# Performance work log

Hardware: AMD Instinct MI355X
Metric: run time of the kernel (lower is better)

The kernel has to match this reference:

```python
import jax, jax.numpy as jnp
import numpy as np

B, T, D_IN, D = 32, 40, 1024, 400


def _offset(level, length):
    return level * length - level * (level - 1) // 2


def _unit(h):
    return h / (jnp.linalg.norm(h, axis=-1, keepdims=True) + 1e-8)


def _inside_index(length):
    idx = {}
    for level in range(1, length):
        L = length - level
        li = np.zeros((L, level), np.int32)
        ri = np.zeros((L, level), np.int32)
        for pos in range(L):
            for k in range(level):
                li[pos, k] = _offset(k, length) + pos
                ri[pos, k] = _offset(level - k - 1, length) + pos + k + 1
        idx[level] = (li, ri)
    return idx


def _outside_index(length):
    idx = {}
    for level in range(length - 2, -1, -1):
        L = length - level
        N = length - level - 1
        pi = np.zeros((L, N), np.int32)
        si = np.zeros((L, N), np.int32)
        for pos in range(L):
            c = 0
            for j in range(pos):  # sibling on the left of this span
                pi[pos, c] = _offset(level + j + 1, length) + pos - j - 1
                si[pos, c] = _offset(j, length) + pos - j - 1
                c += 1
            for j in range(L - 1 - pos):  # sibling on the right
                pi[pos, c] = _offset(level + j + 1, length) + pos
                si[pos, c] = _offset(j, length) + pos + level + 1
                c += 1
        idx[level] = (pi, si)
    return idx


def _diora_forward(x, W_leaf, b_leaf, W_in, b_in, S_in, W_out, b_out, S_out, root_h):
    Bb, length, _ = x.shape
    size = W_leaf.shape[1]
    ncells = length * (length + 1) // 2
    in_idx = _inside_index(length)
    out_idx = _outside_index(length)

    h_in = jnp.zeros((Bb, ncells, size), x.dtype)
    s_in = jnp.zeros((Bb, ncells), x.dtype)
    h_out = jnp.zeros((Bb, ncells, size), x.dtype)
    s_out = jnp.zeros((Bb, ncells), x.dtype)

    # leaf transform + unit normalize (level 0 of inside chart)
    leaf = _unit(jax.nn.relu(x @ W_leaf + b_leaf))
    h_in = h_in.at[:, :length].set(leaf)

    # inside pass: bottom-up CKY levels
    for level in range(1, length):
        L = length - level
        off = _offset(level, length)
        li, ri = in_idx[level]
        hl = h_in[:, li]  # [B, L, level, D]
        hr = h_in[:, ri]
        hc = jax.nn.relu(jnp.einsum('blkd,df->blkf', jnp.concatenate([hl, hr], -1), W_in) + b_in)
        sb = jnp.einsum('blkd,de,blke->blk', hl, S_in, hr) + s_in[:, li] + s_in[:, ri]
        p = jax.nn.softmax(sb, axis=-1)
        h_in = h_in.at[:, off:off + L].set(_unit(jnp.einsum('blk,blkd->bld', p, hc)))
        s_in = s_in.at[:, off:off + L].set(jnp.sum(p * sb, axis=-1))

    # outside pass: root init then top-down
    root = _unit(root_h)[None, None, :]
    h_out = h_out.at[:, -1:].set(jnp.broadcast_to(root, (Bb, 1, size)))
    for level in range(length - 2, -1, -1):
        L = length - level
        off = _offset(level, length)
        pi, si = out_idx[level]
        hp = h_out[:, pi]  # [B, L, N, D] parent outside
        hs = h_in[:, si]   # [B, L, N, D] sibling inside
        hc = jax.nn.relu(jnp.einsum('blnd,df->blnf', jnp.concatenate([hp, hs], -1), W_out) + b_out)
        sb = jnp.einsum('blnd,de,blne->bln', hp, S_out, hs) + s_out[:, pi] + s_in[:, si]
        p = jax.nn.softmax(sb, axis=-1)
        h_out = h_out.at[:, off:off + L].set(_unit(jnp.einsum('bln,blnd->bld', p, hc)))
        s_out = s_out.at[:, off:off + L].set(jnp.sum(p * sb, axis=-1))

    # pack chart: [B, ncells, 2*(D+1)]
    return jnp.concatenate([h_in, s_in[..., None], h_out, s_out[..., None]], axis=-1)


def setup_inputs() -> dict:
    key = jax.random.key(0)
    ks = jax.random.split(key, 10)
    return {
        'x': jax.random.normal(ks[0], (B, T, D_IN), jnp.float32),
        'W_leaf': jax.random.normal(ks[1], (D_IN, D), jnp.float32),
        'b_leaf': jax.random.normal(ks[2], (D,), jnp.float32),
        'W_in': jax.random.normal(ks[3], (2 * D, D), jnp.float32),
        'b_in': jax.random.normal(ks[4], (D,), jnp.float32),
        'S_in': jax.random.normal(ks[5], (D, D), jnp.float32),
        'W_out': jax.random.normal(ks[6], (2 * D, D), jnp.float32),
        'b_out': jax.random.normal(ks[7], (D,), jnp.float32),
        'S_out': jax.random.normal(ks[8], (D, D), jnp.float32),
        'root_h': jax.random.normal(ks[9], (D,), jnp.float32),
    }


def reference(x, W_leaf, b_leaf, W_in, b_in, S_in, W_out, b_out, S_out, root_h):
    return _diora_forward(x, W_leaf, b_leaf, W_in, b_in, S_in, W_out, b_out, S_out, root_h)
```

## Files before the change

### kernel.cpp

```cpp
#include <hip/hip_runtime.h>
#include <hip/hip_bf16.h>
#include <math.h>


#define TLEN 40
#define DD 400
#define NCELL 820
#define STR 802

typedef short bf16x8 __attribute__((ext_vector_type(8)));
typedef float f32x4 __attribute__((ext_vector_type(4)));

__host__ __device__ __forceinline__ int coff(int l) { return l * TLEN - (l * (l - 1)) / 2; }
__device__ __forceinline__ float bf2f(unsigned short u) {
    return __uint_as_float(((unsigned)u) << 16);
}
__device__ __forceinline__ unsigned short f2bf(float v) {
    __hip_bfloat16 h = __float2bfloat16(v);
    return *reinterpret_cast<unsigned short*>(&h);
}

__global__ __launch_bounds__(256)
void prep_weights(const float* __restrict__ Win, const float* __restrict__ Sin,
                  const float* __restrict__ Wout, const float* __restrict__ Sout,
                  const float* __restrict__ Wl,
                  unsigned short* __restrict__ WinT, unsigned short* __restrict__ WoutT,
                  unsigned short* __restrict__ WlT)
{
    int n = blockIdx.x;
    if (n < 2400) {
        const float* src; int col; unsigned short* dst;
        if (n < 1200) {
            dst = WinT + (size_t)n * 400;
            if (n < 400)      { src = Win;             col = n; }
            else if (n < 800) { src = Win + 400 * 400; col = n - 400; }
            else              { src = Sin;             col = n - 800; }
        } else {
            int m = n - 1200;
            dst = WoutT + (size_t)m * 400;
            if (m < 400)      { src = Wout;             col = m; }
            else if (m < 800) { src = Sout;             col = m - 400; }
            else              { src = Wout + 400 * 400; col = m - 800; }
        }
        for (int k = threadIdx.x; k < 400; k += 256)
            dst[k] = f2bf(src[(size_t)k * 400 + col]);
    } else {
        int m = n - 2400;
        unsigned short* dst = WlT + (size_t)m * 1024;
        for (int k = threadIdx.x; k < 1024; k += 256)
            dst[k] = f2bf(Wl[(size_t)k * 400 + m]);
    }
}

__global__ __launch_bounds__(256)
void mgemm(const unsigned short* __restrict__ A, const unsigned short* __restrict__ WT,
           unsigned short* __restrict__ Cb, unsigned short* __restrict__ Cc,
           int M, int N, int L, int cb, int co_b, int nsplit)
{
    __shared__ unsigned short As[64][40];
    __shared__ unsigned short Bs[128][40];
    const int tid = threadIdx.x;
    const int bm = blockIdx.x, bn = blockIdx.y;
    const int w = tid >> 6, lane = tid & 63;
    const int l15 = lane & 15, kb = (lane >> 4) * 8;

    const int ar = tid >> 2, ach = (tid & 3) * 8;
    const int rg = bm * 64 + ar;
    const unsigned short* Ap = nullptr;
    if (rg < M) { int b = rg / L, p = rg - b * L;
                  Ap = A + ((size_t)(b * NCELL) + cb + p) * 400; }

    const int bcol = tid & 127, bh = (tid >> 7) * 16;
    const int ng = bn * 128 + bcol;
    const unsigned short* Bp = (ng < N) ? WT + (size_t)ng * 400 : nullptr;

    f32x4 acc[4][2];
    #pragma unroll
    for (int r = 0; r < 4; ++r)
        #pragma unroll
        for (int c = 0; c < 2; ++c) { f32x4 z = {0.f, 0.f, 0.f, 0.f}; acc[r][c] = z; }

    for (int k0 = 0; k0 < 400; k0 += 32) {
        int4 av = {0, 0, 0, 0};
        if (Ap && (k0 + ach) < 400) av = *(const int4*)(Ap + k0 + ach);
        int4 bv0 = {0, 0, 0, 0}, bv1 = {0, 0, 0, 0};
        if (Bp && (k0 + bh) < 400) {
            bv0 = *(const int4*)(Bp + k0 + bh);
            bv1 = *(const int4*)(Bp + k0 + bh + 8);
        }
        __syncthreads();
        *(int4*)&As[ar][ach] = av;
        *(int4*)&Bs[bcol][bh] = bv0;
        *(int4*)&Bs[bcol][bh + 8] = bv1;
        __syncthreads();

        bf16x8 af[4], bf[2];
        #pragma unroll
        for (int r = 0; r < 4; ++r) af[r] = *(const bf16x8*)&As[r * 16 + l15][kb];
        #pragma unroll
        for (int c = 0; c < 2; ++c) bf[c] = *(const bf16x8*)&Bs[w * 32 + c * 16 + l15][kb];
        #pragma unroll
        for (int r = 0; r < 4; ++r)
            #pragma unroll
            for (int c = 0; c < 2; ++c)
                acc[r][c] = __builtin_amdgcn_mfma_f32_16x16x32_bf16(af[r], bf[c], acc[r][c], 0, 0, 0);
    }

    const int rowb = (lane >> 4) * 4;
    #pragma unroll
    for (int r = 0; r < 4; ++r) {
        #pragma unroll
        for (int c = 0; c < 2; ++c) {
            int gcol = bn * 128 + w * 32 + c * 16 + l15;
            if (gcol >= N) continue;
            #pragma unroll
            for (int reg = 0; reg < 4; ++reg) {
                int rr = bm * 64 + r * 16 + rowb + reg;
                if (rr >= M) continue;
                int b = rr / L, p = rr - b * L;
                size_t cell = (size_t)(b * NCELL) + cb + p;
                unsigned short v = f2bf(acc[r][c][reg]);
                if (gcol < nsplit) Cb[cell * 800 + co_b + gcol] = v;
                else               Cc[cell * 400 + (gcol - nsplit)] = v;
            }
        }
    }
}

__global__ __launch_bounds__(256)
void mleaf(const float* __restrict__ x, const unsigned short* __restrict__ WlT,
           const float* __restrict__ bias, float* __restrict__ leafS)
{
    __shared__ unsigned short As[64][40];
    __shared__ unsigned short Bs[128][40];
    const int tid = threadIdx.x;
    const int bm = blockIdx.x, bn = blockIdx.y;
    const int w = tid >> 6, lane = tid & 63;
    const int l15 = lane & 15, kb = (lane >> 4) * 8;

    const int ar = tid >> 2, ach = (tid & 3) * 8;
    const float* Ap = x + (size_t)(bm * 64 + ar) * 1024;

    const int bcol = tid & 127, bh = (tid >> 7) * 16;
    const int ng = bn * 128 + bcol;
    const unsigned short* Bp = (ng < 400) ? WlT + (size_t)ng * 1024 : nullptr;

    f32x4 acc[4][2];
    #pragma unroll
    for (int r = 0; r < 4; ++r)
        #pragma unroll
        for (int c = 0; c < 2; ++c) { f32x4 z = {0.f, 0.f, 0.f, 0.f}; acc[r][c] = z; }

    for (int k0 = 0; k0 < 1024; k0 += 32) {
        float4 p0 = *(const float4*)(Ap + k0 + ach);
        float4 p1 = *(const float4*)(Ap + k0 + ach + 4);
        unsigned short av[8];
        av[0] = f2bf(p0.x); av[1] = f2bf(p0.y); av[2] = f2bf(p0.z); av[3] = f2bf(p0.w);
        av[4] = f2bf(p1.x); av[5] = f2bf(p1.y); av[6] = f2bf(p1.z); av[7] = f2bf(p1.w);
        int4 bv0 = {0, 0, 0, 0}, bv1 = {0, 0, 0, 0};
        if (Bp) {
            bv0 = *(const int4*)(Bp + k0 + bh);
            bv1 = *(const int4*)(Bp + k0 + bh + 8);
        }
        __syncthreads();
        *(int4*)&As[ar][ach] = *(const int4*)av;
        *(int4*)&Bs[bcol][bh] = bv0;
        *(int4*)&Bs[bcol][bh + 8] = bv1;
        __syncthreads();

        bf16x8 af[4], bf[2];
        #pragma unroll
        for (int r = 0; r < 4; ++r) af[r] = *(const bf16x8*)&As[r * 16 + l15][kb];
        #pragma unroll
        for (int c = 0; c < 2; ++c) bf[c] = *(const bf16x8*)&Bs[w * 32 + c * 16 + l15][kb];
        #pragma unroll
        for (int r = 0; r < 4; ++r)
            #pragma unroll
            for (int c = 0; c < 2; ++c)
                acc[r][c] = __builtin_amdgcn_mfma_f32_16x16x32_bf16(af[r], bf[c], acc[r][c], 0, 0, 0);
    }

    const int rowb = (lane >> 4) * 4;
    #pragma unroll
    for (int r = 0; r < 4; ++r) {
        #pragma unroll
        for (int c = 0; c < 2; ++c) {
            int gcol = bn * 128 + w * 32 + c * 16 + l15;
            if (gcol >= 400) continue;
            float bv = bias[gcol];
            #pragma unroll
            for (int reg = 0; reg < 4; ++reg) {
                int rr = bm * 64 + r * 16 + rowb + reg;
                leafS[(size_t)rr * 400 + gcol] = fmaxf(acc[r][c][reg] + bv, 0.f);
            }
        }
    }
}

__global__ __launch_bounds__(256)
void unit_leaf(float* obuf, const float* __restrict__ leafS, unsigned short* __restrict__ hHin)
{
    int w = threadIdx.x >> 6, lane = threadIdx.x & 63;
    int r = blockIdx.x * 4 + w;
    int b = r / TLEN, pos = r - b * TLEN;
    const float* t = leafS + (size_t)r * 400;
    float ss = 0.f;
    for (int f = lane; f < DD; f += 64) { float v = t[f]; ss += v * v; }
    #pragma unroll
    for (int o = 32; o; o >>= 1) ss += __shfl_xor(ss, o);
    float rinv = 1.f / (sqrtf(ss) + 1e-8f);
    size_t orow = ((size_t)b * NCELL + pos) * STR;
    size_t hrow = ((size_t)b * NCELL + pos) * 400;
    for (int f = lane; f < DD; f += 64) {
        float v = t[f] * rinv;
        obuf[orow + f] = v;
        hHin[hrow + f] = f2bf(v);
    }
    if (lane == 0) obuf[orow + DD] = 0.f;
}

template<int INSIDE>
__global__ __launch_bounds__(256)
void compose_kernel(int lv, float* obuf, const unsigned short* __restrict__ hAB,
                    const unsigned short* __restrict__ hCb,
                    const unsigned short* __restrict__ hHin,
                    unsigned short* __restrict__ hHw,
                    const float* __restrict__ bias)
{
    const int nk  = INSIDE ? lv : (TLEN - 1 - lv);
    const int b   = blockIdx.x & 31;
    const int pos = blockIdx.x >> 5;
    const int cell = coff(lv) + pos;
    const int tid = threadIdx.x;
    const int sA  = INSIDE ? DD : (STR - 1);

    __shared__ int   o1s[TLEN], o2s[TLEN], c1s[TLEN], h2s[TLEN], q1s[TLEN], q2s[TLEN];
    __shared__ float sbs[TLEN], ps[TLEN];
    __shared__ float bsh[DD];
    __shared__ float hnew[DD];
    __shared__ float red[4];
    __shared__ float sh_snew;

    if (tid < nk) {
        int k = tid, i1, i2;
        if (INSIDE) {
            i1 = coff(k) + pos;
            i2 = coff(lv - k - 1) + pos + k + 1;
        } else {
            if (k < pos) { i1 = coff(lv + k + 1) + pos - k - 1; i2 = coff(k) + pos - k - 1; }
            else         { int j = k - pos; i1 = coff(lv + j + 1) + pos; i2 = coff(j) + pos + lv + 1; }
        }
        o1s[k] = (b * NCELL + i1) * 800;
        o2s[k] = (b * NCELL + i2) * 800 + 400;
        c1s[k] = (b * NCELL + i1) * 400;
        h2s[k] = (b * NCELL + i2) * 400;
        q1s[k] = (b * NCELL + i1) * STR;
        q2s[k] = (b * NCELL + i2) * STR;
    }
    for (int f = tid; f < DD; f += 256) bsh[f] = bias[f];
    __syncthreads();

    {
        const int g = tid >> 4, gl = tid & 15;
        for (int k = g; k < nk; k += 16) {
            const unsigned short* v1 = hCb + c1s[k];
            const unsigned short* v2 = hHin + h2s[k];
            float acc = 0.f;
            for (int j = gl * 4; j < 400; j += 64) {
                ushort4 a = *(const ushort4*)(v1 + j);
                ushort4 c = *(const ushort4*)(v2 + j);
                acc += bf2f(a.x) * bf2f(c.x) + bf2f(a.y) * bf2f(c.y)
                     + bf2f(a.z) * bf2f(c.z) + bf2f(a.w) * bf2f(c.w);
            }
            acc += __shfl_xor(acc, 8);
            acc += __shfl_xor(acc, 4);
            acc += __shfl_xor(acc, 2);
            acc += __shfl_xor(acc, 1);
            if (gl == 0)
                sbs[k] = acc + obuf[q1s[k] + sA] + obuf[q2s[k] + DD];
        }
    }
    __syncthreads();

    if (tid < 64) {
        float v = (tid < nk) ? sbs[tid] : -INFINITY;
        float m = v;
        #pragma unroll
        for (int o = 32; o; o >>= 1) m = fmaxf(m, __shfl_xor(m, o));
        float e = (tid < nk) ? __expf(v - m) : 0.f;
        float s = e;
        #pragma unroll
        for (int o = 32; o; o >>= 1) s += __shfl_xor(s, o);
        float p = e / s;
        if (tid < nk) ps[tid] = p;
        float pv = (tid < nk) ? p * v : 0.f;
        #pragma unroll
        for (int o = 32; o; o >>= 1) pv += __shfl_xor(pv, o);
        if (tid == 0) sh_snew = pv;
    }
    __syncthreads();

    if (tid < 200) {
        const int f = 2 * tid;
        const float bf0 = bsh[f], bf1 = bsh[f + 1];
        float ax = 0.f, ay = 0.f;
        #pragma unroll 4
        for (int k = 0; k < nk; ++k) {
            ushort2 a = *(const ushort2*)(hAB + o1s[k] + f);
            ushort2 c = *(const ushort2*)(hAB + o2s[k] + f);
            float p = ps[k];
            ax += p * fmaxf(bf2f(a.x) + bf2f(c.x) + bf0, 0.f);
            ay += p * fmaxf(bf2f(a.y) + bf2f(c.y) + bf1, 0.f);
        }
        hnew[f] = ax; hnew[f + 1] = ay;
    }
    __syncthreads();

    float ss = 0.f;
    for (int f = tid; f < DD; f += 256) { float v = hnew[f]; ss += v * v; }
    #pragma unroll
    for (int o = 32; o; o >>= 1) ss += __shfl_xor(ss, o);
    if ((tid & 63) == 0) red[tid >> 6] = ss;
    __syncthreads();
    float rinv = 1.f / (sqrtf(red[0] + red[1] + red[2] + red[3]) + 1e-8f);

    const int hoff = INSIDE ? 0 : (DD + 1);
    const int soff = INSIDE ? DD : (STR - 1);
    size_t orow = ((size_t)(b * NCELL) + cell) * STR;
    size_t hrow = ((size_t)(b * NCELL) + cell) * 400;
    for (int f = tid; f < DD; f += 256) {
        float v = hnew[f] * rinv;
        obuf[orow + hoff + f] = v;
        hHw[hrow + f] = f2bf(v);
    }
    if (tid == 0) obuf[orow + soff] = sh_snew;
}

__global__ __launch_bounds__(256)
void root_trans(const float* __restrict__ rooth, const float* __restrict__ Wout,
                const float* __restrict__ Sout,
                unsigned short* __restrict__ hAB, unsigned short* __restrict__ hCb)
{
    const int tid = threadIdx.x;
    __shared__ float u[DD];
    __shared__ float red[4];
    __shared__ float part[4][64];
    float ss = 0.f;
    for (int f = tid; f < DD; f += 256) { float v = rooth[f]; ss += v * v; }
    #pragma unroll
    for (int o = 32; o; o >>= 1) ss += __shfl_xor(ss, o);
    if ((tid & 63) == 0) red[tid >> 6] = ss;
    __syncthreads();
    float rinv = 1.f / (sqrtf(red[0] + red[1] + red[2] + red[3]) + 1e-8f);
    for (int f = tid; f < DD; f += 256) u[f] = rooth[f] * rinv;
    __syncthreads();

    const int w = tid >> 6, lane = tid & 63;
    const int n = blockIdx.x * 64 + lane;
    float acc = 0.f;
    if (n < 800) {
        int mat = n / DD;
        const float* Mp = mat ? Sout : Wout;
        int c = n - mat * DD;
        #pragma unroll 4
        for (int k = w * 100; k < w * 100 + 100; ++k) acc += u[k] * Mp[(size_t)k * DD + c];
    }
    part[w][lane] = acc;
    __syncthreads();
    if (w == 0 && n < 800) {
        float v = part[0][lane] + part[1][lane] + part[2][lane] + part[3][lane];
        unsigned short bv = f2bf(v);
        if (n < 400) {
            for (int b = 0; b < 32; ++b)
                hAB[((size_t)b * NCELL + NCELL - 1) * 800 + n] = bv;
        } else {
            for (int b = 0; b < 32; ++b)
                hCb[((size_t)b * NCELL + NCELL - 1) * 400 + (n - 400)] = bv;
        }
    }
}

__global__ __launch_bounds__(256)
void root_write(const float* __restrict__ rooth, float* obuf)
{
    const int b = blockIdx.x;
    const int tid = threadIdx.x;
    __shared__ float red[4];
    float ss = 0.f;
    for (int f = tid; f < DD; f += 256) { float v = rooth[f]; ss += v * v; }
    #pragma unroll
    for (int o = 32; o; o >>= 1) ss += __shfl_xor(ss, o);
    if ((tid & 63) == 0) red[tid >> 6] = ss;
    __syncthreads();
    float rinv = 1.f / (sqrtf(red[0] + red[1] + red[2] + red[3]) + 1e-8f);
    size_t orow = ((size_t)b * NCELL + NCELL - 1) * STR;
    for (int f = tid; f < DD; f += 256) obuf[orow + DD + 1 + f] = rooth[f] * rinv;
    if (tid == 0) obuf[orow + STR - 1] = 0.f;
}

extern "C" void kernel_launch(void* const* d_in, const int* in_sizes, int n_in,
                              void* d_out, int out_size, void* d_ws, size_t ws_size,
                              hipStream_t stream)
{
    const float* x     = (const float*)d_in[0];
    const float* Wl    = (const float*)d_in[1];
    const float* blf   = (const float*)d_in[2];
    const float* Win   = (const float*)d_in[3];
    const float* bin   = (const float*)d_in[4];
    const float* Sin   = (const float*)d_in[5];
    const float* Wout  = (const float*)d_in[6];
    const float* bout  = (const float*)d_in[7];
    const float* Sout  = (const float*)d_in[8];
    const float* rooth = (const float*)d_in[9];

    float* obuf = (float*)d_out;
    unsigned short* hAB   = (unsigned short*)d_ws;
    unsigned short* hCb   = hAB   + (size_t)32 * NCELL * 800;
    unsigned short* hHin  = hCb   + (size_t)32 * NCELL * 400;
    unsigned short* hHout = hHin  + (size_t)32 * NCELL * 400;
    unsigned short* WinT  = hHout + (size_t)32 * NCELL * 400;
    unsigned short* WoutT = WinT  + (size_t)1200 * 400;
    unsigned short* WlT   = WoutT + (size_t)1200 * 400;
    float* leafS = (float*)(WlT + (size_t)400 * 1024);

    prep_weights<<<2800, 256, 0, stream>>>(Win, Sin, Wout, Sout, Wl, WinT, WoutT, WlT);

    mleaf<<<dim3(20, 4), 256, 0, stream>>>(x, WlT, blf, leafS);
    unit_leaf<<<320, 256, 0, stream>>>(obuf, leafS, hHin);

    for (int lv = 0; lv < TLEN; ++lv) {
        int L = TLEN - lv;
        int cb = coff(lv);
        if (lv > 0)
            compose_kernel<1><<<L * 32, 256, 0, stream>>>(lv, obuf, hAB, hCb, hHin, hHin, bin);
        if (lv < TLEN - 1) {
            int M = L * 32;
            dim3 g((M + 63) / 64, 10);
            mgemm<<<g, 256, 0, stream>>>(hHin, WinT, hAB, hCb, M, 1200, L, cb, 0, 800);
        }
    }

    {
        dim3 g(410, 4);
        mgemm<<<g, 256, 0, stream>>>(hHin, WoutT + (size_t)800 * 400, hAB, hCb,
                                     32 * NCELL, 400, NCELL, 0, 400, 400);
    }
    root_trans<<<13, 256, 0, stream>>>(rooth, Wout, Sout, hAB, hCb);
    root_write<<<32, 256, 0, stream>>>(rooth, obuf);

    for (int lv = TLEN - 2; lv >= 0; --lv) {
        int L = TLEN - lv;
        int cb = coff(lv);
        compose_kernel<0><<<L * 32, 256, 0, stream>>>(lv, obuf, hAB, hCb, hHin, hHout, bout);
        if (lv > 0) {
            int M = L * 32;
            dim3 g((M + 63) / 64, 7);
            mgemm<<<g, 256, 0, stream>>>(hHout, WoutT, hAB, hCb, M, 800, L, cb, 0, 400);
        }
    }
}
```

Measured before the change: 2.142 ms.

## Fuse outside-sibling projection into inside GEMMs, widen K-tile, prefetch compose operands

The outside-pass sibling projection (Wout lower half applied to inside states) is folded into the per-level inside GEMM as a third output segment written to a new hBout buffer. This removes the separate full-chart GEMM. The GEMM K-tile doubles from 32 to 64, so there are fewer barriers per tile at the cost of more LDS. The compose kernel now prefetches the first 8 child rows into shared memory while the score reduction runs, and root_write is merged into root_trans. These changes add an extra workspace buffer and raise per-block register and LDS pressure.

Result: slower. 3.825 ms (+78.6%).

```diff
diff --git a/kernel.cpp b/kernel.cpp
--- a/kernel.cpp
+++ b/kernel.cpp
@@ -24,24 +24,24 @@
 void prep_weights(const float* __restrict__ Win, const float* __restrict__ Sin,
                   const float* __restrict__ Wout, const float* __restrict__ Sout,
                   const float* __restrict__ Wl,
-                  unsigned short* __restrict__ WinT, unsigned short* __restrict__ WoutT,
+                  unsigned short* __restrict__ WinX, unsigned short* __restrict__ WoutT,
                   unsigned short* __restrict__ WlT)
 {
     int n = blockIdx.x;
-    if (n < 2400) {
-        const float* src; int col; unsigned short* dst;
-        if (n < 1200) {
-            dst = WinT + (size_t)n * 400;
-            if (n < 400)      { src = Win;             col = n; }
-            else if (n < 800) { src = Win + 400 * 400; col = n - 400; }
-            else              { src = Sin;             col = n - 800; }
-        } else {
-            int m = n - 1200;
-            dst = WoutT + (size_t)m * 400;
-            if (m < 400)      { src = Wout;             col = m; }
-            else if (m < 800) { src = Sout;             col = m - 400; }
-            else              { src = Wout + 400 * 400; col = m - 800; }
-        }
+    if (n < 1600) {
+        const float* src; int col;
+        if (n < 400)       { src = Win;              col = n; }
+        else if (n < 800)  { src = Win + 400 * 400;  col = n - 400; }
+        else if (n < 1200) { src = Sin;              col = n - 800; }
+        else               { src = Wout + 400 * 400; col = n - 1200; }
+        unsigned short* dst = WinX + (size_t)n * 400;
+        for (int k = threadIdx.x; k < 400; k += 256)
+            dst[k] = f2bf(src[(size_t)k * 400 + col]);
+    } else if (n < 2400) {
+        int m = n - 1600;
+        const float* src = (m < 400) ? Wout : Sout;
+        int col = (m < 400) ? m : m - 400;
+        unsigned short* dst = WoutT + (size_t)m * 400;
         for (int k = threadIdx.x; k < 400; k += 256)
             dst[k] = f2bf(src[(size_t)k * 400 + col]);
     } else {
@@ -55,24 +55,34 @@
 __global__ __launch_bounds__(256)
 void mgemm(const unsigned short* __restrict__ A, const unsigned short* __restrict__ WT,
            unsigned short* __restrict__ Cb, unsigned short* __restrict__ Cc,
-           int M, int N, int L, int cb, int co_b, int nsplit)
-{
-    __shared__ unsigned short As[64][40];
-    __shared__ unsigned short Bs[128][40];
+           unsigned short* __restrict__ Cd,
+           int M, int N, int L, int cb, int ns1, int ns2)
+{
+    __shared__ unsigned short As[64][72];
+    __shared__ unsigned short Bs[128][72];
     const int tid = threadIdx.x;
     const int bm = blockIdx.x, bn = blockIdx.y;
     const int w = tid >> 6, lane = tid & 63;
     const int l15 = lane & 15, kb = (lane >> 4) * 8;
 
-    const int ar = tid >> 2, ach = (tid & 3) * 8;
-    const int rg = bm * 64 + ar;
-    const unsigned short* Ap = nullptr;
-    if (rg < M) { int b = rg / L, p = rg - b * L;
-                  Ap = A + ((size_t)(b * NCELL) + cb + p) * 400; }
-
-    const int bcol = tid & 127, bh = (tid >> 7) * 16;
-    const int ng = bn * 128 + bcol;
-    const unsigned short* Bp = (ng < N) ? WT + (size_t)ng * 400 : nullptr;
+    int arow[2] = { tid >> 3, (tid + 256) >> 3 };
+    const int akc = (tid & 7) * 8;
+    const unsigned short* Aps[2];
+    #pragma unroll
+    for (int i = 0; i < 2; ++i) {
+        int rg = bm * 64 + arow[i];
+        if (rg < M) { int b = rg / L, p = rg - b * L;
+                      Aps[i] = A + ((size_t)(b * NCELL) + cb + p) * 400; }
+        else Aps[i] = nullptr;
+    }
+    int bcol[4];
+    const unsigned short* Bps[4];
+    #pragma unroll
+    for (int i = 0; i < 4; ++i) {
+        bcol[i] = (tid + i * 256) >> 3;
+        int ng = bn * 128 + bcol[i];
+        Bps[i] = (ng < N) ? WT + (size_t)ng * 400 : nullptr;
+    }
 
     f32x4 acc[4][2];
     #pragma unroll
@@ -80,30 +90,39 @@
         #pragma unroll
         for (int c = 0; c < 2; ++c) { f32x4 z = {0.f, 0.f, 0.f, 0.f}; acc[r][c] = z; }
 
-    for (int k0 = 0; k0 < 400; k0 += 32) {
-        int4 av = {0, 0, 0, 0};
-        if (Ap && (k0 + ach) < 400) av = *(const int4*)(Ap + k0 + ach);
-        int4 bv0 = {0, 0, 0, 0}, bv1 = {0, 0, 0, 0};
-        if (Bp && (k0 + bh) < 400) {
-            bv0 = *(const int4*)(Bp + k0 + bh);
-            bv1 = *(const int4*)(Bp + k0 + bh + 8);
+    for (int k0 = 0; k0 < 400; k0 += 64) {
+        int4 av[2], bv[4];
+        #pragma unroll
+        for (int i = 0; i < 2; ++i) {
+            int4 z = {0, 0, 0, 0};
+            av[i] = (Aps[i] && (k0 + akc) < 400) ? *(const int4*)(Aps[i] + k0 + akc) : z;
+        }
+        #pragma unroll
+        for (int i = 0; i < 4; ++i) {
+            int4 z = {0, 0, 0, 0};
+            bv[i] = (Bps[i] && (k0 + akc) < 400) ? *(const int4*)(Bps[i] + k0 + akc) : z;
         }
         __syncthreads();
-        *(int4*)&As[ar][ach] = av;
-        *(int4*)&Bs[bcol][bh] = bv0;
-        *(int4*)&Bs[bcol][bh + 8] = bv1;
+        #pragma unroll
+        for (int i = 0; i < 2; ++i) *(int4*)&As[arow[i]][akc] = av[i];
+        #pragma unroll
+        for (int i = 0; i < 4; ++i) *(int4*)&Bs[bcol[i]][akc] = bv[i];
         __syncthreads();
 
-        bf16x8 af[4], bf[2];
-        #pragma unroll
-        for (int r = 0; r < 4; ++r) af[r] = *(const bf16x8*)&As[r * 16 + l15][kb];
-        #pragma unroll
-        for (int c = 0; c < 2; ++c) bf[c] = *(const bf16x8*)&Bs[w * 32 + c * 16 + l15][kb];
-        #pragma unroll
-        for (int r = 0; r < 4; ++r)
+        #pragma unroll
+        for (int ks = 0; ks < 64; ks += 32) {
+            if (k0 + ks >= 400) break;
+            bf16x8 af[4], bf[2];
             #pragma unroll
-            for (int c = 0; c < 2; ++c)
-                acc[r][c] = __builtin_amdgcn_mfma_f32_16x16x32_bf16(af[r], bf[c], acc[r][c], 0, 0, 0);
+            for (int r = 0; r < 4; ++r) af[r] = *(const bf16x8*)&As[r * 16 + l15][ks + kb];
+            #pragma unroll
+            for (int c = 0; c < 2; ++c) bf[c] = *(const bf16x8*)&Bs[w * 32 + c * 16 + l15][ks + kb];
+            #pragma unroll
+            for (int r = 0; r < 4; ++r)
+                #pragma unroll
+                for (int c = 0; c < 2; ++c)
+                    acc[r][c] = __builtin_amdgcn_mfma_f32_16x16x32_bf16(af[r], bf[c], acc[r][c], 0, 0, 0);
+        }
     }
 
     const int rowb = (lane >> 4) * 4;
@@ -120,8 +139,9 @@
                 int b = rr / L, p = rr - b * L;
                 size_t cell = (size_t)(b * NCELL) + cb + p;
                 unsigned short v = f2bf(acc[r][c][reg]);
-                if (gcol < nsplit) Cb[cell * 800 + co_b + gcol] = v;
-                else               Cc[cell * 400 + (gcol - nsplit)] = v;
+                if (gcol < ns1)      Cb[cell * 800 + gcol] = v;
+                else if (gcol < ns2) Cc[cell * 400 + (gcol - ns1)] = v;
+                else                 Cd[cell * 400 + (gcol - ns2)] = v;
             }
         }
     }
@@ -222,6 +242,7 @@
 template<int INSIDE>
 __global__ __launch_bounds__(256)
 void compose_kernel(int lv, float* obuf, const unsigned short* __restrict__ hAB,
+                    const unsigned short* __restrict__ hBp, int bstr,
                     const unsigned short* __restrict__ hCb,
                     const unsigned short* __restrict__ hHin,
                     unsigned short* __restrict__ hHw,
@@ -240,6 +261,8 @@
     __shared__ float hnew[DD];
     __shared__ float red[4];
     __shared__ float sh_snew;
+    __shared__ unsigned short pfA[8][408];
+    __shared__ unsigned short pfB[8][408];
 
     if (tid < nk) {
         int k = tid, i1, i2;
@@ -251,7 +274,7 @@
             else         { int j = k - pos; i1 = coff(lv + j + 1) + pos; i2 = coff(j) + pos + lv + 1; }
         }
         o1s[k] = (b * NCELL + i1) * 800;
-        o2s[k] = (b * NCELL + i2) * 800 + 400;
+        o2s[k] = (b * NCELL + i2) * bstr;
         c1s[k] = (b * NCELL + i1) * 400;
         h2s[k] = (b * NCELL + i2) * 400;
         q1s[k] = (b * NCELL + i1) * STR;
@@ -259,6 +282,19 @@
     }
     for (int f = tid; f < DD; f += 256) bsh[f] = bias[f];
     __syncthreads();
+
+    const int nk0 = (nk < 8) ? nk : 8;
+    const int npfc = nk0 * 100;
+    int4 pfv[4]; int pfid[4]; int npf = 0;
+    for (int c = tid; c < npfc; c += 256) {
+        int arr = (c >= nk0 * 50) ? 1 : 0;
+        int rem = c - arr * nk0 * 50;
+        int k = rem / 50, off = (rem - k * 50) * 8;
+        const unsigned short* src = arr ? (hBp + o2s[k] + off) : (hAB + o1s[k] + off);
+        pfv[npf] = *(const int4*)src;
+        pfid[npf] = c;
+        npf++;
+    }
 
     {
         const int g = tid >> 4, gl = tid & 15;
@@ -282,6 +318,16 @@
     }
     __syncthreads();
 
+    for (int i = 0; i < npf; ++i) {
+        int c = pfid[i];
+        int arr = (c >= nk0 * 50) ? 1 : 0;
+        int rem = c - arr * nk0 * 50;
+        int k = rem / 50, off = (rem - k * 50) * 8;
+        unsigned short* dst = (arr ? pfB[k] : pfA[k]) + off;
+        *(int4*)dst = pfv[i];
+    }
+    __syncthreads();
+
     if (tid < 64) {
         float v = (tid < nk) ? sbs[tid] : -INFINITY;
         float m = v;
@@ -304,10 +350,17 @@
         const int f = 2 * tid;
         const float bf0 = bsh[f], bf1 = bsh[f + 1];
         float ax = 0.f, ay = 0.f;
+        for (int k = 0; k < nk0; ++k) {
+            ushort2 a = *(const ushort2*)&pfA[k][f];
+            ushort2 c = *(const ushort2*)&pfB[k][f];
+            float p = ps[k];
+            ax += p * fmaxf(bf2f(a.x) + bf2f(c.x) + bf0, 0.f);
+            ay += p * fmaxf(bf2f(a.y) + bf2f(c.y) + bf1, 0.f);
+        }
         #pragma unroll 4
-        for (int k = 0; k < nk; ++k) {
+        for (int k = nk0; k < nk; ++k) {
             ushort2 a = *(const ushort2*)(hAB + o1s[k] + f);
-            ushort2 c = *(const ushort2*)(hAB + o2s[k] + f);
+            ushort2 c = *(const ushort2*)(hBp + o2s[k] + f);
             float p = ps[k];
             ax += p * fmaxf(bf2f(a.x) + bf2f(c.x) + bf0, 0.f);
             ay += p * fmaxf(bf2f(a.y) + bf2f(c.y) + bf1, 0.f);
@@ -339,7 +392,8 @@
 __global__ __launch_bounds__(256)
 void root_trans(const float* __restrict__ rooth, const float* __restrict__ Wout,
                 const float* __restrict__ Sout,
-                unsigned short* __restrict__ hAB, unsigned short* __restrict__ hCb)
+                unsigned short* __restrict__ hAB, unsigned short* __restrict__ hCb,
+                float* obuf)
 {
     const int tid = threadIdx.x;
     __shared__ float u[DD];
@@ -366,6 +420,12 @@
         for (int k = w * 100; k < w * 100 + 100; ++k) acc += u[k] * Mp[(size_t)k * DD + c];
     }
     part[w][lane] = acc;
+    if (w == 1 && n < 400) {
+        for (int b = 0; b < 32; ++b)
+            obuf[((size_t)b * NCELL + NCELL - 1) * STR + DD + 1 + n] = u[n];
+    }
+    if (w == 2 && blockIdx.x == 0 && lane < 32)
+        obuf[((size_t)lane * NCELL + NCELL - 1) * STR + (STR - 1)] = 0.f;
     __syncthreads();
     if (w == 0 && n < 800) {
         float v = part[0][lane] + part[1][lane] + part[2][lane] + part[3][lane];
@@ -378,24 +438,6 @@
                 hCb[((size_t)b * NCELL + NCELL - 1) * 400 + (n - 400)] = bv;
         }
     }
-}
-
-__global__ __launch_bounds__(256)
-void root_write(const float* __restrict__ rooth, float* obuf)
-{
-    const int b = blockIdx.x;
-    const int tid = threadIdx.x;
-    __shared__ float red[4];
-    float ss = 0.f;
-    for (int f = tid; f < DD; f += 256) { float v = rooth[f]; ss += v * v; }
-    #pragma unroll
-    for (int o = 32; o; o >>= 1) ss += __shfl_xor(ss, o);
-    if ((tid & 63) == 0) red[tid >> 6] = ss;
-    __syncthreads();
-    float rinv = 1.f / (sqrtf(red[0] + red[1] + red[2] + red[3]) + 1e-8f);
-    size_t orow = ((size_t)b * NCELL + NCELL - 1) * STR;
-    for (int f = tid; f < DD; f += 256) obuf[orow + DD + 1 + f] = rooth[f] * rinv;
-    if (tid == 0) obuf[orow + STR - 1] = 0.f;
 }
 
 extern "C" void kernel_launch(void* const* d_in, const int* in_sizes, int n_in,
@@ -414,16 +456,18 @@
     const float* rooth = (const float*)d_in[9];
 
     float* obuf = (float*)d_out;
+    const size_t CELLS = (size_t)32 * NCELL;
     unsigned short* hAB   = (unsigned short*)d_ws;
-    unsigned short* hCb   = hAB   + (size_t)32 * NCELL * 800;
-    unsigned short* hHin  = hCb   + (size_t)32 * NCELL * 400;
-    unsigned short* hHout = hHin  + (size_t)32 * NCELL * 400;
-    unsigned short* WinT  = hHout + (size_t)32 * NCELL * 400;
-    unsigned short* WoutT = WinT  + (size_t)1200 * 400;
-    unsigned short* WlT   = WoutT + (size_t)1200 * 400;
+    unsigned short* hCb   = hAB   + CELLS * 800;
+    unsigned short* hHin  = hCb   + CELLS * 400;
+    unsigned short* hHout = hHin  + CELLS * 400;
+    unsigned short* hBout = hHout + CELLS * 400;
+    unsigned short* WinX  = hBout + CELLS * 400;
+    unsigned short* WoutT = WinX  + (size_t)1600 * 400;
+    unsigned short* WlT   = WoutT + (size_t)800 * 400;
     float* leafS = (float*)(WlT + (size_t)400 * 1024);
 
-    prep_weights<<<2800, 256, 0, stream>>>(Win, Sin, Wout, Sout, Wl, WinT, WoutT, WlT);
+    prep_weights<<<2800, 256, 0, stream>>>(Win, Sin, Wout, Sout, Wl, WinX, WoutT, WlT);
 
     mleaf<<<dim3(20, 4), 256, 0, stream>>>(x, WlT, blf, leafS);
     unit_leaf<<<320, 256, 0, stream>>>(obuf, leafS, hHin);
@@ -432,30 +476,28 @@
         int L = TLEN - lv;
         int cb = coff(lv);
         if (lv > 0)
-            compose_kernel<1><<<L * 32, 256, 0, stream>>>(lv, obuf, hAB, hCb, hHin, hHin, bin);
+            compose_kernel<1><<<L * 32, 256, 0, stream>>>(lv, obuf, hAB, hAB + 400, 800,
+                                                          hCb, hHin, hHin, bin);
         if (lv < TLEN - 1) {
             int M = L * 32;
-            dim3 g((M + 63) / 64, 10);
-            mgemm<<<g, 256, 0, stream>>>(hHin, WinT, hAB, hCb, M, 1200, L, cb, 0, 800);
-        }
-    }
-
-    {
-        dim3 g(410, 4);
-        mgemm<<<g, 256, 0, stream>>>(hHin, WoutT + (size_t)800 * 400, hAB, hCb,
-                                     32 * NCELL, 400, NCELL, 0, 400, 400);
-    }
-    root_trans<<<13, 256, 0, stream>>>(rooth, Wout, Sout, hAB, hCb);
-    root_write<<<32, 256, 0, stream>>>(rooth, obuf);
+            dim3 g((M + 63) / 64, 13);
+            mgemm<<<g, 256, 0, stream>>>(hHin, WinX, hAB, hCb, hBout,
+                                         M, 1600, L, cb, 800, 1200);
+        }
+    }
+
+    root_trans<<<13, 256, 0, stream>>>(rooth, Wout, Sout, hAB, hCb, obuf);
 
     for (int lv = TLEN - 2; lv >= 0; --lv) {
         int L = TLEN - lv;
         int cb = coff(lv);
-        compose_kernel<0><<<L * 32, 256, 0, stream>>>(lv, obuf, hAB, hCb, hHin, hHout, bout);
+        compose_kernel<0><<<L * 32, 256, 0, stream>>>(lv, obuf, hAB, hBout, 400,
+                                                      hCb, hHin, hHout, bout);
         if (lv > 0) {
             int M = L * 32;
             dim3 g((M + 63) / 64, 7);
-            mgemm<<<g, 256, 0, stream>>>(hHout, WoutT, hAB, hCb, M, 800, L, cb, 0, 400);
-        }
-    }
-}
+            mgemm<<<g, 256, 0, stream>>>(hHout, WoutT, hAB, hCb, hBout,
+                                         M, 800, L, cb, 400, 800);
+        }
+    }
+}
```
